# Performance work log

Measured on AMD Instinct MI355X. Metric: run time of the kernel, lower is better.

## Reference

```python
import jax, jax.numpy as jnp
import numpy as np
import math

B, H, S, D = 2, 16, 2048, 64

def setup_inputs() -> dict:
    key = jax.random.key(0)
    kq, kk, kv = jax.random.split(key, 3)
    Q = jax.random.normal(kq, (B, H, S, D), dtype=jnp.float32)
    K = jax.random.normal(kk, (B, H, S, D), dtype=jnp.float32)
    V = jax.random.normal(kv, (B, H, S, D), dtype=jnp.float32)
    causal_mask = jnp.tril(jnp.ones((S, S), dtype=bool))
    return {"Q": Q, "K": K, "V": V, "causal_mask": causal_mask}

def reference(Q, K, V, causal_mask):
    d_k = K.shape[-1]
    scores = jnp.einsum('bhqd,bhkd->bhqk', Q, K) / math.sqrt(d_k)
    scores = jnp.where(causal_mask, scores, -jnp.inf)
    probs = jax.nn.softmax(scores, axis=-1)
    return jnp.einsum('bhqk,bhkd->bhqd', probs, V)
```

## Files before the change

kernel.cpp:

```cpp
#include <hip/hip_runtime.h>
#include <math.h>


constexpr int kS   = 2048;
constexpr int kD   = 64;
constexpr int kBH  = 32;
constexpr int kPadP = 72;
constexpr int kFragBH = 64 * 4 * 512;

typedef short short8 __attribute__((ext_vector_type(8)));
typedef float float4v __attribute__((ext_vector_type(4)));
typedef float float16v __attribute__((ext_vector_type(16)));
typedef unsigned int u32;
typedef unsigned short u16;

static __device__ inline u16 f2bf(float f) {
  union { float f; unsigned u; } v; v.f = f;
  unsigned r = v.u + 0x7FFF + ((v.u >> 16) & 1);
  return (u16)(r >> 16);
}

static __device__ inline short8 pack8(float4v a, float4v b) {
  short8 r;
  r[0] = (short)f2bf(a[0]); r[1] = (short)f2bf(a[1]);
  r[2] = (short)f2bf(a[2]); r[3] = (short)f2bf(a[3]);
  r[4] = (short)f2bf(b[0]); r[5] = (short)f2bf(b[1]);
  r[6] = (short)f2bf(b[2]); r[7] = (short)f2bf(b[3]);
  return r;
}

static __device__ inline void swap32(u32 a, u32 b, u32& oa, u32& ob) {
#if __has_builtin(__builtin_amdgcn_permlane32_swap)
  auto r = __builtin_amdgcn_permlane32_swap(a, b, false, false);
  oa = r[0]; ob = r[1];
#else
  asm volatile("v_permlane32_swap_b32 %0, %1" : "+v"(a), "+v"(b));
  oa = a; ob = b;
#endif
}

__global__ __launch_bounds__(256)
void prep_kernel(const float* __restrict__ Q, const float* __restrict__ K,
                 const float* __restrict__ V,
                 u16* __restrict__ Qf, u16* __restrict__ Kf, u16* __restrict__ Vf) {
  __shared__ u16 tile[64 * kPadP];
  const int tid = threadIdx.x;
  const int bh = blockIdx.y, st = blockIdx.x;
  const size_t ibase = (size_t)bh * kS * kD + (size_t)st * 64 * kD;
  const size_t fbase = (size_t)bh * kFragBH;
  const int r  = tid >> 2;
  const int c0 = (tid & 3) * 16;
  const int dk = tid & 3;
  const int U  = st * 2 + (r >> 5);
  const int lr = r & 31;
  {
    const float scl = 0.125f * 1.44269504089f;
    const float* qp = Q + ibase + (size_t)r * kD + c0;
    float4v a = *(const float4v*)(qp);
    float4v b = *(const float4v*)(qp + 4);
    float4v c = *(const float4v*)(qp + 8);
    float4v d = *(const float4v*)(qp + 12);
    #pragma unroll
    for (int i = 0; i < 4; ++i) { a[i] *= scl; b[i] *= scl; c[i] *= scl; d[i] *= scl; }
    u16* dst = Qf + fbase + (size_t)(U * 4 + dk) * 512;
    *(short8*)(dst + lr * 8)        = pack8(a, b);
    *(short8*)(dst + (32 + lr) * 8) = pack8(c, d);
  }
  {
    const float* kp = K + ibase + (size_t)r * kD + c0;
    float4v a = *(const float4v*)(kp);
    float4v b = *(const float4v*)(kp + 4);
    float4v c = *(const float4v*)(kp + 8);
    float4v d = *(const float4v*)(kp + 12);
    u16* dst = Kf + fbase + (size_t)(U * 4 + dk) * 512;
    *(short8*)(dst + lr * 8)        = pack8(a, b);
    *(short8*)(dst + (32 + lr) * 8) = pack8(c, d);
  }
  {
    const float* vp = V + ibase + (size_t)r * kD + c0;
    float4v a = *(const float4v*)(vp);
    float4v b = *(const float4v*)(vp + 4);
    float4v c = *(const float4v*)(vp + 8);
    float4v d = *(const float4v*)(vp + 12);
    u16* t = &tile[r * kPadP + c0];
    *(short8*)t       = pack8(a, b);
    *(short8*)(t + 8) = pack8(c, d);
  }
  __syncthreads();
  {
    const int dd = tid >> 2;
    const int s0 = (tid & 3) * 16;
    short8 w0, w1;
    #pragma unroll
    for (int i = 0; i < 8; ++i) {
      w0[i] = (short)tile[(s0 + i) * kPadP + dd];
      w1[i] = (short)tile[(s0 + 8 + i) * kPadP + dd];
    }
    const int ku   = st * 2 + (s0 >> 5);
    const int koff = s0 & 31;
    const int c    = ((koff >> 4) << 1) | (dd >> 5);
    u16* vdst = Vf + fbase + (size_t)(ku * 4 + c) * 512;
    *(short8*)(vdst + (dd & 31) * 8)        = w0;
    *(short8*)(vdst + (32 + (dd & 31)) * 8) = w1;
  }
}

__global__ __launch_bounds__(256, 4)
void fattn_kernel(const u16* __restrict__ Qf, const u16* __restrict__ Kf,
                  const u16* __restrict__ Vf, float* __restrict__ O) {
  __shared__ u32   ldsP[5][32][33];
  __shared__ float ldsL[5][32];

  const int tid  = threadIdx.x;
  const int wave = tid >> 6;
  const int lane = tid & 63;
  const int l31  = lane & 31;
  const int h    = lane >> 5;

  const int blk = blockIdx.x;
  const int bh  = (blk & 7) * 4 + ((blk >> 3) & 3);
  const int sA  = blk >> 5;
  const int sB  = 63 - sA;
  const int t   = sB + 1;
  const int lo  = (65 * wave) >> 2;
  const int hi  = (65 * (wave + 1)) >> 2;
  const int uT  = min(max(t, lo), hi);

  const size_t fb = (size_t)bh * kFragBH;
  const u16* gk = Kf + fb + lane * 8;
  const u16* gv = Vf + fb + lane * 8;

  float16v zf;
  #pragma unroll
  for (int i = 0; i < 16; ++i) zf[i] = 0.f;

  float16v acc0 = zf, acc1 = zf;
  float lac = 0.f;
  short8 qf[4];

  auto loadQ = [&](int s) {
    const u16* qp = Qf + fb + (size_t)(s * 4) * 512 + lane * 8;
    #pragma unroll
    for (int dk = 0; dk < 4; ++dk) qf[dk] = *(const short8*)(qp + dk * 512);
  };

  auto unitCompute = [&](int k, int sdiag) {
    const u16* kp = gk + (size_t)k * 2048;
    const u16* vp = gv + (size_t)k * 2048;
    short8 kf[4], vf[4];
    #pragma unroll
    for (int i = 0; i < 4; ++i) kf[i] = *(const short8*)(kp + i * 512);
    #pragma unroll
    for (int i = 0; i < 4; ++i) vf[i] = *(const short8*)(vp + i * 512);

    __builtin_amdgcn_s_setprio(1);
    float16v sv = __builtin_amdgcn_mfma_f32_32x32x16_bf16(kf[0], qf[0], zf, 0, 0, 0);
    sv = __builtin_amdgcn_mfma_f32_32x32x16_bf16(kf[1], qf[1], sv, 0, 0, 0);
    sv = __builtin_amdgcn_mfma_f32_32x32x16_bf16(kf[2], qf[2], sv, 0, 0, 0);
    sv = __builtin_amdgcn_mfma_f32_32x32x16_bf16(kf[3], qf[3], sv, 0, 0, 0);
    __builtin_amdgcn_s_setprio(0);

    if (k == sdiag) {
      const int qg = sdiag * 32 + l31;
      #pragma unroll
      for (int r = 0; r < 16; ++r) {
        const int kg = k * 32 + (r & 3) + 8 * (r >> 2) + 4 * h;
        if (kg > qg) sv[r] = -1e30f;
      }
    }

    u32 pk[8];
    #pragma unroll
    for (int g2 = 0; g2 < 4; ++g2) {
      const u32 u0 = __float_as_uint(__builtin_amdgcn_exp2f(sv[4 * g2 + 0]));
      const u32 u1 = __float_as_uint(__builtin_amdgcn_exp2f(sv[4 * g2 + 1]));
      const u32 u2 = __float_as_uint(__builtin_amdgcn_exp2f(sv[4 * g2 + 2]));
      const u32 u3 = __float_as_uint(__builtin_amdgcn_exp2f(sv[4 * g2 + 3]));
      pk[2 * g2]     = __builtin_amdgcn_perm(u1, u0, 0x07060302u);
      pk[2 * g2 + 1] = __builtin_amdgcn_perm(u3, u2, 0x07060302u);
    }

    {
      float e0 = 0.f, e1 = 0.f;
      #pragma unroll
      for (int i = 0; i < 4; ++i) {
        e0 += __uint_as_float(pk[i] << 16)     + __uint_as_float(pk[i] & 0xFFFF0000u);
        e1 += __uint_as_float(pk[i + 4] << 16) + __uint_as_float(pk[i + 4] & 0xFFFF0000u);
      }
      lac += e0 + e1;
    }

    union { u32 u[4]; short8 s8; } pf;
    swap32(pk[0], pk[2], pf.u[0], pf.u[2]);
    swap32(pk[1], pk[3], pf.u[1], pf.u[3]);
    __builtin_amdgcn_s_setprio(1);
    acc0 = __builtin_amdgcn_mfma_f32_32x32x16_bf16(pf.s8, vf[0], acc0, 0, 0, 0);
    acc1 = __builtin_amdgcn_mfma_f32_32x32x16_bf16(pf.s8, vf[1], acc1, 0, 0, 0);
    __builtin_amdgcn_s_setprio(0);
    swap32(pk[4], pk[6], pf.u[0], pf.u[2]);
    swap32(pk[5], pk[7], pf.u[1], pf.u[3]);
    __builtin_amdgcn_s_setprio(1);
    acc0 = __builtin_amdgcn_mfma_f32_32x32x16_bf16(pf.s8, vf[2], acc0, 0, 0, 0);
    acc1 = __builtin_amdgcn_mfma_f32_32x32x16_bf16(pf.s8, vf[3], acc1, 0, 0, 0);
    __builtin_amdgcn_s_setprio(0);
  };

  auto dump = [&](int slot) {
    #pragma unroll
    for (int r = 0; r < 16; ++r) {
      const int row = (r & 3) + 8 * (r >> 2) + 4 * h;
      ldsP[slot][row][l31] = (u32)f2bf(acc0[r]) | ((u32)f2bf(acc1[r]) << 16);
    }
    const float lt = lac + __shfl_xor(lac, 32);
    if (lane < 32) ldsL[slot][lane] = lt;
  };

  if (lo < uT) {
    loadQ(sB);
    for (int u = lo; u < uT; ++u) unitCompute(u, sB);
    dump(wave);
    acc0 = zf; acc1 = zf; lac = 0.f;
  }
  if (uT < hi) {
    loadQ(sA);
    for (int u = uT; u < hi; ++u) unitCompute(u - t, sA);
    dump((lo < uT) ? 4 : wave);
  }

  __syncthreads();

  {
    const int setid = tid >> 7;
    const int sOut  = setid ? sA : sB;
    const bool v0 = setid ? (0  >= t) : (0  < t);
    const bool v1 = setid ? (16 >= t) : (16 < t);
    const bool v2 = setid ? (32 >= t) : (32 < t);
    const bool v3 = setid ? (48 >= t) : (48 < t);
    const bool v4 = (setid != 0) && (t != 48);

    const int q  = (tid & 127) >> 2;
    const int c0 = (tid & 3) * 8;

    float lsum = 0.f;
    if (v0) lsum += ldsL[0][q];
    if (v1) lsum += ldsL[1][q];
    if (v2) lsum += ldsL[2][q];
    if (v3) lsum += ldsL[3][q];
    if (v4) lsum += ldsL[4][q];
    const float inv = 1.f / lsum;

    float* op = O + ((size_t)bh * kS + sOut * 32 + q) * kD;
    #pragma unroll
    for (int i = 0; i < 8; ++i) {
      const int c = c0 + i;
      float lov = 0.f, hiv = 0.f;
      if (v0) { const u32 p = ldsP[0][q][c]; lov += __uint_as_float(p << 16); hiv += __uint_as_float(p & 0xFFFF0000u); }
      if (v1) { const u32 p = ldsP[1][q][c]; lov += __uint_as_float(p << 16); hiv += __uint_as_float(p & 0xFFFF0000u); }
      if (v2) { const u32 p = ldsP[2][q][c]; lov += __uint_as_float(p << 16); hiv += __uint_as_float(p & 0xFFFF0000u); }
      if (v3) { const u32 p = ldsP[3][q][c]; lov += __uint_as_float(p << 16); hiv += __uint_as_float(p & 0xFFFF0000u); }
      if (v4) { const u32 p = ldsP[4][q][c]; lov += __uint_as_float(p << 16); hiv += __uint_as_float(p & 0xFFFF0000u); }
      op[c]      = lov * inv;
      op[c + 32] = hiv * inv;
    }
  }
}

extern "C" void kernel_launch(void* const* d_in, const int* in_sizes, int n_in,
                              void* d_out, int out_size, void* d_ws, size_t ws_size,
                              hipStream_t stream) {
  const float* Q = (const float*)d_in[0];
  const float* K = (const float*)d_in[1];
  const float* V = (const float*)d_in[2];
  float* O = (float*)d_out;

  const size_t nKV = (size_t)kBH * kS * kD;
  u16* Qf = (u16*)d_ws;
  u16* Kf = Qf + nKV;
  u16* Vf = Kf + nKV;

  dim3 gprep(kS / 64, kBH);
  prep_kernel<<<gprep, 256, 0, stream>>>(Q, K, V, Qf, Kf, Vf);
  fattn_kernel<<<1024, 256, 0, stream>>>(Qf, Kf, Vf, O);
}
```

Before: 137.0 us.

## Software-pipeline K/V fragment loads with double-buffered K and manual vmcnt waits

Replaces the per-unit blocking loads of K and V fragments with inline-asm global loads, double-buffering K so the next unit's K is prefetched while the current one computes. Explicit s_waitcnt vmcnt counters and sched barriers let the V load overlap the QK MFMA and exp work. Launch bounds occupancy drops from 4 to 3 to leave room for the extra live registers. Relies on exact outstanding-load counting; any compiler-inserted global load would break the vmcnt accounting.

New measurement: 137.4 us. About the same (+0.3%).

```diff
diff --git a/kernel.cpp b/kernel.cpp
--- a/kernel.cpp
+++ b/kernel.cpp
@@ -12,6 +12,7 @@
 typedef float float4v __attribute__((ext_vector_type(4)));
 typedef float float16v __attribute__((ext_vector_type(16)));
 typedef unsigned int u32;
+typedef unsigned int u32x4 __attribute__((ext_vector_type(4)));
 typedef unsigned short u16;
 
 static __device__ inline u16 f2bf(float f) {
@@ -37,6 +38,13 @@
   asm volatile("v_permlane32_swap_b32 %0, %1" : "+v"(a), "+v"(b));
   oa = a; ob = b;
 #endif
+}
+
+static __device__ inline void gload16(u32x4& d, const u16* p) {
+  asm volatile("global_load_dwordx4 %0, %1, off" : "=v"(d) : "v"(p));
+}
+static __device__ inline short8 asfrag(u32x4 u) {
+  union { u32x4 u; short8 s; } c; c.u = u; return c.s;
 }
 
 __global__ __launch_bounds__(256)
@@ -105,7 +113,7 @@
   }
 }
 
-__global__ __launch_bounds__(256, 4)
+__global__ __launch_bounds__(256, 3)
 void fattn_kernel(const u16* __restrict__ Qf, const u16* __restrict__ Kf,
                   const u16* __restrict__ Vf, float* __restrict__ O) {
   __shared__ u32   ldsP[5][32][33];
@@ -137,27 +145,38 @@
   float16v acc0 = zf, acc1 = zf;
   float lac = 0.f;
   short8 qf[4];
-
-  auto loadQ = [&](int s) {
-    const u16* qp = Qf + fb + (size_t)(s * 4) * 512 + lane * 8;
-    #pragma unroll
-    for (int dk = 0; dk < 4; ++dk) qf[dk] = *(const short8*)(qp + dk * 512);
-  };
-
-  auto unitCompute = [&](int k, int sdiag) {
-    const u16* kp = gk + (size_t)k * 2048;
-    const u16* vp = gv + (size_t)k * 2048;
-    short8 kf[4], vf[4];
-    #pragma unroll
-    for (int i = 0; i < 4; ++i) kf[i] = *(const short8*)(kp + i * 512);
-    #pragma unroll
-    for (int i = 0; i < 4; ++i) vf[i] = *(const short8*)(vp + i * 512);
+  u32x4 kX[4], kY[4], vX[4];
+
+  auto issueK = [&](u32x4* buf, int k) {
+    const u16* p = gk + (size_t)k * 2048;
+    gload16(buf[0], p);
+    gload16(buf[1], p + 512);
+    gload16(buf[2], p + 1024);
+    gload16(buf[3], p + 1536);
+  };
+  auto issueV = [&](int k) {
+    const u16* p = gv + (size_t)k * 2048;
+    gload16(vX[0], p);
+    gload16(vX[1], p + 512);
+    gload16(vX[2], p + 1024);
+    gload16(vX[3], p + 1536);
+  };
+
+  auto unit = [&](u32x4* kc, u32x4* kn, int k, int kend, int sdiag) {
+    issueV(k);
+    if (k < kend) {
+      issueK(kn, k + 1);
+      asm volatile("s_waitcnt vmcnt(8)" ::: "memory");
+    } else {
+      asm volatile("s_waitcnt vmcnt(4)" ::: "memory");
+    }
+    __builtin_amdgcn_sched_barrier(0);
 
     __builtin_amdgcn_s_setprio(1);
-    float16v sv = __builtin_amdgcn_mfma_f32_32x32x16_bf16(kf[0], qf[0], zf, 0, 0, 0);
-    sv = __builtin_amdgcn_mfma_f32_32x32x16_bf16(kf[1], qf[1], sv, 0, 0, 0);
-    sv = __builtin_amdgcn_mfma_f32_32x32x16_bf16(kf[2], qf[2], sv, 0, 0, 0);
-    sv = __builtin_amdgcn_mfma_f32_32x32x16_bf16(kf[3], qf[3], sv, 0, 0, 0);
+    float16v sv = __builtin_amdgcn_mfma_f32_32x32x16_bf16(asfrag(kc[0]), qf[0], zf, 0, 0, 0);
+    sv = __builtin_amdgcn_mfma_f32_32x32x16_bf16(asfrag(kc[1]), qf[1], sv, 0, 0, 0);
+    sv = __builtin_amdgcn_mfma_f32_32x32x16_bf16(asfrag(kc[2]), qf[2], sv, 0, 0, 0);
+    sv = __builtin_amdgcn_mfma_f32_32x32x16_bf16(asfrag(kc[3]), qf[3], sv, 0, 0, 0);
     __builtin_amdgcn_s_setprio(0);
 
     if (k == sdiag) {
@@ -190,19 +209,39 @@
       lac += e0 + e1;
     }
 
+    if (k < kend) asm volatile("s_waitcnt vmcnt(4)" ::: "memory");
+    else          asm volatile("s_waitcnt vmcnt(0)" ::: "memory");
+    __builtin_amdgcn_sched_barrier(0);
+
     union { u32 u[4]; short8 s8; } pf;
     swap32(pk[0], pk[2], pf.u[0], pf.u[2]);
     swap32(pk[1], pk[3], pf.u[1], pf.u[3]);
     __builtin_amdgcn_s_setprio(1);
-    acc0 = __builtin_amdgcn_mfma_f32_32x32x16_bf16(pf.s8, vf[0], acc0, 0, 0, 0);
-    acc1 = __builtin_amdgcn_mfma_f32_32x32x16_bf16(pf.s8, vf[1], acc1, 0, 0, 0);
+    acc0 = __builtin_amdgcn_mfma_f32_32x32x16_bf16(pf.s8, asfrag(vX[0]), acc0, 0, 0, 0);
+    acc1 = __builtin_amdgcn_mfma_f32_32x32x16_bf16(pf.s8, asfrag(vX[1]), acc1, 0, 0, 0);
     __builtin_amdgcn_s_setprio(0);
     swap32(pk[4], pk[6], pf.u[0], pf.u[2]);
     swap32(pk[5], pk[7], pf.u[1], pf.u[3]);
     __builtin_amdgcn_s_setprio(1);
-    acc0 = __builtin_amdgcn_mfma_f32_32x32x16_bf16(pf.s8, vf[2], acc0, 0, 0, 0);
-    acc1 = __builtin_amdgcn_mfma_f32_32x32x16_bf16(pf.s8, vf[3], acc1, 0, 0, 0);
+    acc0 = __builtin_amdgcn_mfma_f32_32x32x16_bf16(pf.s8, asfrag(vX[2]), acc0, 0, 0, 0);
+    acc1 = __builtin_amdgcn_mfma_f32_32x32x16_bf16(pf.s8, asfrag(vX[3]), acc1, 0, 0, 0);
     __builtin_amdgcn_s_setprio(0);
+  };
+
+  auto runPhase = [&](int s, int kb, int ke) {
+    const u16* qp = Qf + fb + (size_t)(s * 4) * 512 + lane * 8;
+    #pragma unroll
+    for (int dk = 0; dk < 4; ++dk) qf[dk] = *(const short8*)(qp + dk * 512);
+    asm volatile("s_waitcnt vmcnt(0)" ::: "memory");
+    __builtin_amdgcn_sched_barrier(0);
+
+    const int kend = ke - 1;
+    issueK(kX, kb);
+    int k = kb;
+    for (;;) {
+      unit(kX, kY, k, kend, s); if (++k == ke) break;
+      unit(kY, kX, k, kend, s); if (++k == ke) break;
+    }
   };
 
   auto dump = [&](int slot) {
@@ -216,14 +255,12 @@
   };
 
   if (lo < uT) {
-    loadQ(sB);
-    for (int u = lo; u < uT; ++u) unitCompute(u, sB);
+    runPhase(sB, lo, uT);
     dump(wave);
     acc0 = zf; acc1 = zf; lac = 0.f;
   }
   if (uT < hi) {
-    loadQ(sA);
-    for (int u = uT; u < hi; ++u) unitCompute(u - t, sA);
+    runPhase(sA, uT - t, hi - t);
     dump((lo < uT) ? 4 : wave);
   }
 
```

## Process two query tiles per block sharing K/V loads; convert Q inline

Applied to the files above, without the earlier changes.

Each block now handles a pair of adjacent 32-row query tiles for each causal half, so every K/V fragment loaded from global memory feeds two QK/PV computations. The grid is halved to 512 blocks, launch bounds drop to 2 blocks per SM, and LDS partial buffers double. Q is no longer pre-converted by the prep kernel. Instead it is scaled and packed to bf16 directly in the attention kernel, which removes one workspace write and read. The trade-offs are higher register pressure and fewer blocks to spread across the device.

New measurement: 144.6 us. 5.5% more time.

```diff
diff --git a/kernel.cpp b/kernel.cpp
--- a/kernel.cpp
+++ b/kernel.cpp
@@ -40,9 +40,8 @@
 }
 
 __global__ __launch_bounds__(256)
-void prep_kernel(const float* __restrict__ Q, const float* __restrict__ K,
-                 const float* __restrict__ V,
-                 u16* __restrict__ Qf, u16* __restrict__ Kf, u16* __restrict__ Vf) {
+void prep_kernel(const float* __restrict__ K, const float* __restrict__ V,
+                 u16* __restrict__ Kf, u16* __restrict__ Vf) {
   __shared__ u16 tile[64 * kPadP];
   const int tid = threadIdx.x;
   const int bh = blockIdx.y, st = blockIdx.x;
@@ -54,19 +53,6 @@
   const int U  = st * 2 + (r >> 5);
   const int lr = r & 31;
   {
-    const float scl = 0.125f * 1.44269504089f;
-    const float* qp = Q + ibase + (size_t)r * kD + c0;
-    float4v a = *(const float4v*)(qp);
-    float4v b = *(const float4v*)(qp + 4);
-    float4v c = *(const float4v*)(qp + 8);
-    float4v d = *(const float4v*)(qp + 12);
-    #pragma unroll
-    for (int i = 0; i < 4; ++i) { a[i] *= scl; b[i] *= scl; c[i] *= scl; d[i] *= scl; }
-    u16* dst = Qf + fbase + (size_t)(U * 4 + dk) * 512;
-    *(short8*)(dst + lr * 8)        = pack8(a, b);
-    *(short8*)(dst + (32 + lr) * 8) = pack8(c, d);
-  }
-  {
     const float* kp = K + ibase + (size_t)r * kD + c0;
     float4v a = *(const float4v*)(kp);
     float4v b = *(const float4v*)(kp + 4);
@@ -105,11 +91,11 @@
   }
 }
 
-__global__ __launch_bounds__(256, 4)
-void fattn_kernel(const u16* __restrict__ Qf, const u16* __restrict__ Kf,
+__global__ __launch_bounds__(256, 2)
+void fattn_kernel(const float* __restrict__ Qp, const u16* __restrict__ Kf,
                   const u16* __restrict__ Vf, float* __restrict__ O) {
-  __shared__ u32   ldsP[5][32][33];
-  __shared__ float ldsL[5][32];
+  __shared__ u32   ldsP[5][2][32][33];
+  __shared__ float ldsL[5][2][32];
 
   const int tid  = threadIdx.x;
   const int wave = tid >> 6;
@@ -119,40 +105,38 @@
 
   const int blk = blockIdx.x;
   const int bh  = (blk & 7) * 4 + ((blk >> 3) & 3);
-  const int sA  = blk >> 5;
-  const int sB  = 63 - sA;
-  const int t   = sB + 1;
-  const int lo  = (65 * wave) >> 2;
-  const int hi  = (65 * (wave + 1)) >> 2;
-  const int uT  = min(max(t, lo), hi);
-
-  const size_t fb = (size_t)bh * kFragBH;
-  const u16* gk = Kf + fb + lane * 8;
-  const u16* gv = Vf + fb + lane * 8;
+  const int pp  = blk >> 5;
+  const int tP  = 2 * pp + 2;
+  const int lo  = (66 * wave) >> 2;
+  const int hi  = (66 * (wave + 1)) >> 2;
+  const int uT  = min(max(tP, lo), hi);
+
+  const u16* gk = Kf + (size_t)bh * kFragBH + lane * 8;
+  const u16* gv = Vf + (size_t)bh * kFragBH + lane * 8;
 
   float16v zf;
   #pragma unroll
   for (int i = 0; i < 16; ++i) zf[i] = 0.f;
 
-  float16v acc0 = zf, acc1 = zf;
-  float lac = 0.f;
-  short8 qf[4];
-
-  auto loadQ = [&](int s) {
-    const u16* qp = Qf + fb + (size_t)(s * 4) * 512 + lane * 8;
-    #pragma unroll
-    for (int dk = 0; dk < 4; ++dk) qf[dk] = *(const short8*)(qp + dk * 512);
-  };
-
-  auto unitCompute = [&](int k, int sdiag) {
-    const u16* kp = gk + (size_t)k * 2048;
-    const u16* vp = gv + (size_t)k * 2048;
-    short8 kf[4], vf[4];
-    #pragma unroll
-    for (int i = 0; i < 4; ++i) kf[i] = *(const short8*)(kp + i * 512);
-    #pragma unroll
-    for (int i = 0; i < 4; ++i) vf[i] = *(const short8*)(vp + i * 512);
-
+  float16v acc00 = zf, acc01 = zf, acc10 = zf, acc11 = zf;
+  float lac0 = 0.f, lac1 = 0.f;
+  short8 qf0[4], qf1[4];
+
+  auto loadQ = [&](int s, short8* qf) {
+    const float scl = 0.125f * 1.44269504089f;
+    const float* qp = Qp + ((size_t)bh * kS + (size_t)(s * 32 + l31)) * kD + h * 8;
+    #pragma unroll
+    for (int dk = 0; dk < 4; ++dk) {
+      float4v a = *(const float4v*)(qp + dk * 16);
+      float4v b = *(const float4v*)(qp + dk * 16 + 4);
+      #pragma unroll
+      for (int i = 0; i < 4; ++i) { a[i] *= scl; b[i] *= scl; }
+      qf[dk] = pack8(a, b);
+    }
+  };
+
+  auto process = [&](const short8* qf, float16v& a0, float16v& a1, float& lac,
+                     int sdiag, int k, const short8* kf, const short8* vf) {
     __builtin_amdgcn_s_setprio(1);
     float16v sv = __builtin_amdgcn_mfma_f32_32x32x16_bf16(kf[0], qf[0], zf, 0, 0, 0);
     sv = __builtin_amdgcn_mfma_f32_32x32x16_bf16(kf[1], qf[1], sv, 0, 0, 0);
@@ -160,7 +144,7 @@
     sv = __builtin_amdgcn_mfma_f32_32x32x16_bf16(kf[3], qf[3], sv, 0, 0, 0);
     __builtin_amdgcn_s_setprio(0);
 
-    if (k == sdiag) {
+    if (k >= sdiag) {
       const int qg = sdiag * 32 + l31;
       #pragma unroll
       for (int r = 0; r < 16; ++r) {
@@ -194,71 +178,88 @@
     swap32(pk[0], pk[2], pf.u[0], pf.u[2]);
     swap32(pk[1], pk[3], pf.u[1], pf.u[3]);
     __builtin_amdgcn_s_setprio(1);
-    acc0 = __builtin_amdgcn_mfma_f32_32x32x16_bf16(pf.s8, vf[0], acc0, 0, 0, 0);
-    acc1 = __builtin_amdgcn_mfma_f32_32x32x16_bf16(pf.s8, vf[1], acc1, 0, 0, 0);
+    a0 = __builtin_amdgcn_mfma_f32_32x32x16_bf16(pf.s8, vf[0], a0, 0, 0, 0);
+    a1 = __builtin_amdgcn_mfma_f32_32x32x16_bf16(pf.s8, vf[1], a1, 0, 0, 0);
     __builtin_amdgcn_s_setprio(0);
     swap32(pk[4], pk[6], pf.u[0], pf.u[2]);
     swap32(pk[5], pk[7], pf.u[1], pf.u[3]);
     __builtin_amdgcn_s_setprio(1);
-    acc0 = __builtin_amdgcn_mfma_f32_32x32x16_bf16(pf.s8, vf[2], acc0, 0, 0, 0);
-    acc1 = __builtin_amdgcn_mfma_f32_32x32x16_bf16(pf.s8, vf[3], acc1, 0, 0, 0);
+    a0 = __builtin_amdgcn_mfma_f32_32x32x16_bf16(pf.s8, vf[2], a0, 0, 0, 0);
+    a1 = __builtin_amdgcn_mfma_f32_32x32x16_bf16(pf.s8, vf[3], a1, 0, 0, 0);
     __builtin_amdgcn_s_setprio(0);
+  };
+
+  auto unit = [&](int k, int s0, int s1) {
+    const u16* kp = gk + (size_t)k * 2048;
+    const u16* vp = gv + (size_t)k * 2048;
+    short8 kf[4], vf[4];
+    #pragma unroll
+    for (int i = 0; i < 4; ++i) kf[i] = *(const short8*)(kp + i * 512);
+    #pragma unroll
+    for (int i = 0; i < 4; ++i) vf[i] = *(const short8*)(vp + i * 512);
+    process(qf0, acc00, acc01, lac0, s0, k, kf, vf);
+    process(qf1, acc10, acc11, lac1, s1, k, kf, vf);
+  };
+
+  auto runPhase = [&](int p, int kb, int ke) {
+    loadQ(2 * p,     qf0);
+    loadQ(2 * p + 1, qf1);
+    for (int k = kb; k < ke; ++k) unit(k, 2 * p, 2 * p + 1);
   };
 
   auto dump = [&](int slot) {
     #pragma unroll
     for (int r = 0; r < 16; ++r) {
       const int row = (r & 3) + 8 * (r >> 2) + 4 * h;
-      ldsP[slot][row][l31] = (u32)f2bf(acc0[r]) | ((u32)f2bf(acc1[r]) << 16);
-    }
-    const float lt = lac + __shfl_xor(lac, 32);
-    if (lane < 32) ldsL[slot][lane] = lt;
+      ldsP[slot][0][row][l31] = (u32)f2bf(acc00[r]) | ((u32)f2bf(acc01[r]) << 16);
+      ldsP[slot][1][row][l31] = (u32)f2bf(acc10[r]) | ((u32)f2bf(acc11[r]) << 16);
+    }
+    const float lt0 = lac0 + __shfl_xor(lac0, 32);
+    const float lt1 = lac1 + __shfl_xor(lac1, 32);
+    if (lane < 32) { ldsL[slot][0][lane] = lt0; ldsL[slot][1][lane] = lt1; }
   };
 
   if (lo < uT) {
-    loadQ(sB);
-    for (int u = lo; u < uT; ++u) unitCompute(u, sB);
+    runPhase(pp, lo, uT);
     dump(wave);
-    acc0 = zf; acc1 = zf; lac = 0.f;
+    acc00 = zf; acc01 = zf; acc10 = zf; acc11 = zf; lac0 = 0.f; lac1 = 0.f;
   }
   if (uT < hi) {
-    loadQ(sA);
-    for (int u = uT; u < hi; ++u) unitCompute(u - t, sA);
+    runPhase(31 - pp, uT - tP, hi - tP);
     dump((lo < uT) ? 4 : wave);
   }
 
   __syncthreads();
 
   {
-    const int setid = tid >> 7;
-    const int sOut  = setid ? sA : sB;
-    const bool v0 = setid ? (0  >= t) : (0  < t);
-    const bool v1 = setid ? (16 >= t) : (16 < t);
-    const bool v2 = setid ? (32 >= t) : (32 < t);
-    const bool v3 = setid ? (48 >= t) : (48 < t);
-    const bool v4 = (setid != 0) && (t != 48);
-
-    const int q  = (tid & 127) >> 2;
-    const int c0 = (tid & 3) * 8;
+    const int sid     = tid >> 6;
+    const int pairSel = sid >> 1;
+    const int set01   = sid & 1;
+    const int sOut    = pairSel ? (62 - 2 * pp + set01) : (2 * pp + set01);
+    const int j  = tid & 63;
+    const int q  = j >> 1;
+    const int c0 = (j & 1) * 16;
+
+    bool v[5];
+    if (pairSel == 0) { v[0] = true;  v[1] = (tP > 16);  v[2] = false; v[3] = false; v[4] = false; }
+    else              { v[0] = false; v[1] = (tP <= 16); v[2] = true;  v[3] = true;  v[4] = (tP != 16); }
 
     float lsum = 0.f;
-    if (v0) lsum += ldsL[0][q];
-    if (v1) lsum += ldsL[1][q];
-    if (v2) lsum += ldsL[2][q];
-    if (v3) lsum += ldsL[3][q];
-    if (v4) lsum += ldsL[4][q];
+    #pragma unroll
+    for (int s = 0; s < 5; ++s) if (v[s]) lsum += ldsL[s][set01][q];
     const float inv = 1.f / lsum;
 
-    float* op = O + ((size_t)bh * kS + sOut * 32 + q) * kD;
-    #pragma unroll
-    for (int i = 0; i < 8; ++i) {
+    float* op = O + ((size_t)bh * kS + (size_t)(sOut * 32 + q)) * kD;
+    #pragma unroll
+    for (int i = 0; i < 16; ++i) {
       const int c = c0 + i;
       float lov = 0.f, hiv = 0.f;
-      if (v0) { const u32 p = ldsP[0][q][c]; lov += __uint_as_float(p << 16); hiv += __uint_as_float(p & 0xFFFF0000u); }
-      if (v1) { const u32 p = ldsP[1][q][c]; lov += __uint_as_float(p << 16); hiv += __uint_as_float(p & 0xFFFF0000u); }
-      if (v2) { const u32 p = ldsP[2][q][c]; lov += __uint_as_float(p << 16); hiv += __uint_as_float(p & 0xFFFF0000u); }
-      if (v3) { const u32 p = ldsP[3][q][c]; lov += __uint_as_float(p << 16); hiv += __uint_as_float(p & 0xFFFF0000u); }
-      if (v4) { const u32 p = ldsP[4][q][c]; lov += __uint_as_float(p << 16); hiv += __uint_as_float(p & 0xFFFF0000u); }
+      #pragma unroll
+      for (int s = 0; s < 5; ++s) if (v[s]) {
+        const u32 p = ldsP[s][set01][q][c];
+        lov += __uint_as_float(p << 16);
+        hiv += __uint_as_float(p & 0xFFFF0000u);
+      }
       op[c]      = lov * inv;
       op[c + 32] = hiv * inv;
     }
@@ -274,11 +275,10 @@
   float* O = (float*)d_out;
 
   const size_t nKV = (size_t)kBH * kS * kD;
-  u16* Qf = (u16*)d_ws;
-  u16* Kf = Qf + nKV;
+  u16* Kf = (u16*)d_ws;
   u16* Vf = Kf + nKV;
 
   dim3 gprep(kS / 64, kBH);
-  prep_kernel<<<gprep, 256, 0, stream>>>(Q, K, V, Qf, Kf, Vf);
-  fattn_kernel<<<1024, 256, 0, stream>>>(Qf, Kf, Vf, O);
-}
+  prep_kernel<<<gprep, 256, 0, stream>>>(K, V, Kf, Vf);
+  fattn_kernel<<<512, 256, 0, stream>>>(Q, Kf, Vf, O);
+}
```
